# Performance work log

Hardware: AMD Instinct MI355X
Metric: run time of the kernel (lower is better)

Reference implementation:

```python
import jax, jax.numpy as jnp
import numpy as np

N, T, GX, GY, GQ = 16, 64, 256, 256, 256   # solutions, timesteps, source grid, query grid
H, D = 4, 8                                 # attention heads / head dim
SIGMA = 0.2
LY_MIN, LY_MAX = 30.0, 120.0
CU_REF, NI_REF = 0.0029, 0.0018
LX = 100.0


def setup_inputs() -> dict:
    key = jax.random.key(0)
    ks = jax.random.split(key, 7)
    lys = jax.random.uniform(ks[0], (N,), minval=40.0, maxval=110.0)
    ccu = jax.random.uniform(ks[1], (N,), minval=0.001, maxval=CU_REF)
    cni = jax.random.uniform(ks[2], (N,), minval=0.0005, maxval=NI_REF)
    params = jnp.stack([lys, ccu, cni], axis=1).astype(jnp.float32)  # [N,3] raw (Ly, C_Cu, C_Ni)
    x_grids = jnp.tile(jnp.linspace(0.0, LX, GX, dtype=jnp.float32)[None], (N, 1))      # [N,GX]
    y_grids = lys[:, None] * jnp.linspace(0.0, 1.0, GY, dtype=jnp.float32)[None]        # [N,GY]
    c1_src = jax.random.normal(ks[3], (N, T, GX, GY), dtype=jnp.float32)
    c2_src = jax.random.normal(ks[4], (N, T, GX, GY), dtype=jnp.float32)
    Wq_w = 0.1 * jax.random.normal(ks[5], (H * D, 3), dtype=jnp.float32)
    Wk_w = 0.1 * jax.random.normal(ks[6], (H * D, 3), dtype=jnp.float32)
    Wq_b = jnp.zeros((H * D,), jnp.float32)
    Wk_b = jnp.zeros((H * D,), jnp.float32)
    return dict(c1_src=c1_src, c2_src=c2_src, x_grids=x_grids, y_grids=y_grids,
                params=params, Wq_w=Wq_w, Wq_b=Wq_b, Wk_w=Wk_w, Wk_b=Wk_b,
                ly_target=jnp.float32(75.0), c_cu_target=jnp.float32(0.0029),
                c_ni_target=jnp.float32(0.0018))


def _bilinear(c, xg, yg, qx, qy):
    """Linear interp on rectilinear grid, fill_value=0 out of bounds.
    c: [T,Gx,Gy], xg: [Gx], yg: [Gy], qx/qy: [P] -> [T,P]."""
    ix = jnp.clip(jnp.searchsorted(xg, qx, side='right') - 1, 0, xg.shape[0] - 2)
    iy = jnp.clip(jnp.searchsorted(yg, qy, side='right') - 1, 0, yg.shape[0] - 2)
    x0, x1 = xg[ix], xg[ix + 1]
    y0, y1 = yg[iy], yg[iy + 1]
    fx = (qx - x0) / (x1 - x0)
    fy = (qy - y0) / (y1 - y0)
    c00 = c[:, ix, iy]
    c10 = c[:, ix + 1, iy]
    c01 = c[:, ix, iy + 1]
    c11 = c[:, ix + 1, iy + 1]
    v = ((1 - fx) * (1 - fy)) * c00 + (fx * (1 - fy)) * c10 \
        + ((1 - fx) * fy) * c01 + (fx * fy) * c11
    inb = (qx >= xg[0]) & (qx <= xg[-1]) & (qy >= yg[0]) & (qy <= yg[-1])
    return jnp.where(inb[None, :], v, 0.0)


def _forward(c1_src, c2_src, x_grids, y_grids, params, Wq_w, Wq_b, Wk_w, Wk_b,
             ly_target, c_cu_target, c_ni_target):
    # --- parameter normalization (same constants as original) ---
    p = jnp.stack([(params[:, 0] - LY_MIN) / (LY_MAX - LY_MIN),
                   params[:, 1] / CU_REF,
                   params[:, 2] / NI_REF], axis=1)                     # [N,3]
    tgt = jnp.stack([(ly_target - LY_MIN) / (LY_MAX - LY_MIN),
                     c_cu_target / CU_REF,
                     c_ni_target / NI_REF])[None, :]                   # [1,3]
    # --- tiny multi-head attention weights ---
    q = (tgt @ Wq_w.T + Wq_b).reshape(1, H, D)
    k = (p @ Wk_w.T + Wk_b).reshape(p.shape[0], H, D)
    attn = jnp.einsum('nhd,mhd->nmh', k, q) / np.sqrt(D).astype(np.float32)  # [N,1,H]
    attn_w = jax.nn.softmax(attn, axis=0).mean(axis=2).squeeze(1)            # [N]
    # --- gaussian spatial weights ---
    sw = jnp.exp(-0.5 * jnp.sum(((p - tgt) / SIGMA) ** 2, axis=1))
    sw = sw / sw.sum()
    w = attn_w * sw
    w = w / w.sum()
    w = jax.lax.stop_gradient(w)  # original detaches weights before interpolation
    # --- batched bilinear interpolation onto target grid ---
    Lx = x_grids[0, -1]
    unit = jnp.linspace(0.0, 1.0, GQ, dtype=jnp.float32)
    X, Y = jnp.meshgrid(unit * Lx, unit * ly_target, indexing='ij')    # [GQ,GQ]
    qx, qy = X.ravel(), Y.ravel()                                      # [P]
    ys = y_grids * (ly_target / params[:, 0])[:, None]                 # per-solution rescaled Y grids
    interp = jax.vmap(_bilinear, in_axes=(0, 0, 0, None, None))        # -> [N,T,P]
    c1 = jnp.einsum('n,ntp->tp', w, interp(c1_src, x_grids, ys, qx, qy)).reshape(T, GQ, GQ)
    c2 = jnp.einsum('n,ntp->tp', w, interp(c2_src, x_grids, ys, qx, qy)).reshape(T, GQ, GQ)
    # --- boundary conditions ---
    c1 = c1.at[:, :, 0].set(c_cu_target)
    c2 = c2.at[:, :, -1].set(c_ni_target)
    return jnp.stack([c1, c2]), w


def reference(c1_src, c2_src, x_grids, y_grids, params, Wq_w, Wq_b, Wk_w, Wk_b,
              ly_target, c_cu_target, c_ni_target):
    return _forward(c1_src, c2_src, x_grids, y_grids, params, Wq_w, Wq_b, Wk_w, Wk_b,
                    ly_target, c_cu_target, c_ni_target)
```

## Files before the change

### kernel.cpp

```cpp
#include <hip/hip_runtime.h>

#define N_SRC 16
#define T_DIM 64
#define GXD 256
#define GYD 256
#define GQD 256
#define HN 4
#define DN 8
#define TILE_I 16
#define OUT_C_ELEMS (2 * T_DIM * GQD * GQD)

__device__ __forceinline__ float unitv(int i) {
    return (i == GQD - 1) ? 1.0f : (float)i * (1.0f / 255.0f);
}

__global__ void weights_kernel(const float* __restrict__ params,
                               const float* __restrict__ Wq_w, const float* __restrict__ Wq_b,
                               const float* __restrict__ Wk_w, const float* __restrict__ Wk_b,
                               const float* __restrict__ lyt_p, const float* __restrict__ ccut_p,
                               const float* __restrict__ cnit_p,
                               float* __restrict__ out_w) {
    if (threadIdx.x != 0 || blockIdx.x != 0) return;
    const float lyt = *lyt_p, ccut = *ccut_p, cnit = *cnit_p;
    float tgt[3];
    tgt[0] = (lyt - 30.0f) / 90.0f;
    tgt[1] = ccut / 0.0029f;
    tgt[2] = cnit / 0.0018f;
    float q[HN * DN];
    for (int hd = 0; hd < HN * DN; ++hd)
        q[hd] = tgt[0] * Wq_w[hd * 3 + 0] + tgt[1] * Wq_w[hd * 3 + 1] + tgt[2] * Wq_w[hd * 3 + 2] + Wq_b[hd];
    float p[N_SRC][3];
    float attn[N_SRC][HN];
    for (int n = 0; n < N_SRC; ++n) {
        p[n][0] = (params[n * 3 + 0] - 30.0f) / 90.0f;
        p[n][1] = params[n * 3 + 1] / 0.0029f;
        p[n][2] = params[n * 3 + 2] / 0.0018f;
        for (int h = 0; h < HN; ++h) {
            float acc = 0.0f;
            for (int d = 0; d < DN; ++d) {
                int hd = h * DN + d;
                float kv = p[n][0] * Wk_w[hd * 3 + 0] + p[n][1] * Wk_w[hd * 3 + 1] + p[n][2] * Wk_w[hd * 3 + 2] + Wk_b[hd];
                acc += kv * q[hd];
            }
            attn[n][h] = acc / sqrtf(8.0f);
        }
    }
    float aw[N_SRC];
    for (int n = 0; n < N_SRC; ++n) aw[n] = 0.0f;
    for (int h = 0; h < HN; ++h) {
        float m = attn[0][h];
        for (int n = 1; n < N_SRC; ++n) m = fmaxf(m, attn[n][h]);
        float e[N_SRC], s = 0.0f;
        for (int n = 0; n < N_SRC; ++n) { e[n] = expf(attn[n][h] - m); s += e[n]; }
        for (int n = 0; n < N_SRC; ++n) aw[n] += e[n] / s;
    }
    for (int n = 0; n < N_SRC; ++n) aw[n] *= (1.0f / (float)HN);
    float sw[N_SRC], ss = 0.0f;
    for (int n = 0; n < N_SRC; ++n) {
        float d0 = (p[n][0] - tgt[0]) / 0.2f;
        float d1 = (p[n][1] - tgt[1]) / 0.2f;
        float d2 = (p[n][2] - tgt[2]) / 0.2f;
        sw[n] = expf(-0.5f * (d0 * d0 + d1 * d1 + d2 * d2));
        ss += sw[n];
    }
    float w[N_SRC], wsum = 0.0f;
    for (int n = 0; n < N_SRC; ++n) { w[n] = aw[n] * (sw[n] / ss); wsum += w[n]; }
    for (int n = 0; n < N_SRC; ++n) out_w[n] = w[n] / wsum;
}

__global__ __launch_bounds__(256) void fused_kernel(
    const float* __restrict__ c1, const float* __restrict__ c2,
    const float* __restrict__ xg, const float* __restrict__ yg,
    const float* __restrict__ params,
    const float* __restrict__ lyt_p, const float* __restrict__ ccut_p,
    const float* __restrict__ cnit_p,
    const float* __restrict__ wbuf, float* __restrict__ out)
{
    __shared__ float xg_sm[GXD];
    __shared__ float ys_sm[N_SRC][GYD];
    __shared__ float w_sm[N_SRC];

    const int tid = threadIdx.x;
    const int t = blockIdx.y;
    const int i0 = blockIdx.x * TILE_I;
    const float lyt = *lyt_p;

    xg_sm[tid] = xg[tid];
    #pragma unroll
    for (int n = 0; n < N_SRC; ++n) {
        float s = lyt / params[n * 3 + 0];
        ys_sm[n][tid] = yg[n * GYD + tid] * s;
    }
    if (tid < N_SRC) w_sm[tid] = wbuf[tid];
    __syncthreads();

    const int j = tid;
    const float qy = unitv(j) * lyt;
    int iy[N_SRC];
    float wy0[N_SRC], wy1[N_SRC];
    #pragma unroll
    for (int n = 0; n < N_SRC; ++n) {
        int lo = 0, hi = GYD;
        while (lo < hi) { int mid = (lo + hi) >> 1; if (ys_sm[n][mid] <= qy) lo = mid + 1; else hi = mid; }
        int idx = lo - 1;
        idx = idx < 0 ? 0 : (idx > GYD - 2 ? GYD - 2 : idx);
        iy[n] = idx;
        float y0 = ys_sm[n][idx], y1 = ys_sm[n][idx + 1];
        float fy = (qy - y0) / (y1 - y0);
        float vy = (qy >= ys_sm[n][0] && qy <= ys_sm[n][GYD - 1]) ? 1.0f : 0.0f;
        float wn = w_sm[n] * vy;
        wy0[n] = wn * (1.0f - fy);
        wy1[n] = wn * fy;
    }

    const float Lx = xg_sm[GXD - 1];
    const float ccut = *ccut_p, cnit = *cnit_p;

    for (int ii = 0; ii < TILE_I; ++ii) {
        const int i = i0 + ii;
        const float qx = unitv(i) * Lx;
        int lo = 0, hi = GXD;
        while (lo < hi) { int mid = (lo + hi) >> 1; if (xg_sm[mid] <= qx) lo = mid + 1; else hi = mid; }
        int ixi = lo - 1;
        ixi = ixi < 0 ? 0 : (ixi > GXD - 2 ? GXD - 2 : ixi);
        const float x0 = xg_sm[ixi], x1 = xg_sm[ixi + 1];
        const float fx = (qx - x0) / (x1 - x0);
        const float vx = (qx >= xg_sm[0] && qx <= xg_sm[GXD - 1]) ? 1.0f : 0.0f;

        float a10 = 0.0f, a11 = 0.0f, a20 = 0.0f, a21 = 0.0f;
        #pragma unroll
        for (int n = 0; n < N_SRC; ++n) {
            const int base = ((n * T_DIM + t) * GXD + ixi) * GYD + iy[n];
            const float e00 = c1[base],       e01 = c1[base + 1];
            const float e10 = c1[base + GYD], e11 = c1[base + GYD + 1];
            a10 += wy0[n] * e00 + wy1[n] * e01;
            a11 += wy0[n] * e10 + wy1[n] * e11;
            const float f00 = c2[base],       f01 = c2[base + 1];
            const float f10 = c2[base + GYD], f11 = c2[base + GYD + 1];
            a20 += wy0[n] * f00 + wy1[n] * f01;
            a21 += wy0[n] * f10 + wy1[n] * f11;
        }
        float o1 = vx * ((1.0f - fx) * a10 + fx * a11);
        float o2 = vx * ((1.0f - fx) * a20 + fx * a21);
        if (j == 0) o1 = ccut;
        if (j == GQD - 1) o2 = cnit;
        out[(t * GQD + i) * GQD + j] = o1;
        out[((T_DIM + t) * GQD + i) * GQD + j] = o2;
    }
}

extern "C" void kernel_launch(void* const* d_in, const int* in_sizes, int n_in,
                              void* d_out, int out_size, void* d_ws, size_t ws_size,
                              hipStream_t stream) {
    const float* c1     = (const float*)d_in[0];
    const float* c2     = (const float*)d_in[1];
    const float* xg     = (const float*)d_in[2];
    const float* yg     = (const float*)d_in[3];
    const float* params = (const float*)d_in[4];
    const float* Wq_w   = (const float*)d_in[5];
    const float* Wq_b   = (const float*)d_in[6];
    const float* Wk_w   = (const float*)d_in[7];
    const float* Wk_b   = (const float*)d_in[8];
    const float* lyt    = (const float*)d_in[9];
    const float* ccut   = (const float*)d_in[10];
    const float* cnit   = (const float*)d_in[11];
    float* out = (float*)d_out;
    float* out_w = out + OUT_C_ELEMS;

    weights_kernel<<<1, 64, 0, stream>>>(params, Wq_w, Wq_b, Wk_w, Wk_b, lyt, ccut, cnit, out_w);
    dim3 grid(GQD / TILE_I, T_DIM);
    fused_kernel<<<grid, 256, 0, stream>>>(c1, c2, xg, yg, params, lyt, ccut, cnit, out_w, out);
}
```

Measured before the change: 688.6 us.

## Precompute interpolation index/weight tables once and launch one block per output row

Folds the attention-weight computation into a single-block table kernel that also precomputes per-source y indices and weights plus x indices and weights into workspace. The main kernel now reads these tables instead of redoing 16 binary searches per block, and each block handles one output row instead of 16, which gives a larger grid. This removes redundant search work in the gather kernel. In exchange it adds global table reads (16x3 per thread) and depends on workspace being large enough.

Measured after the change: 685.8 us. No clear change (-0.4%).

```diff
diff --git a/kernel.cpp b/kernel.cpp
--- a/kernel.cpp
+++ b/kernel.cpp
@@ -7,82 +7,33 @@
 #define GQD 256
 #define HN 4
 #define DN 8
-#define TILE_I 16
 #define OUT_C_ELEMS (2 * T_DIM * GQD * GQD)
+
+#define WS_IY   0
+#define WS_WY0  16384
+#define WS_WY1  32768
+#define WS_IX   49152
+#define WS_WX0  50176
+#define WS_WX1  51200
 
 __device__ __forceinline__ float unitv(int i) {
     return (i == GQD - 1) ? 1.0f : (float)i * (1.0f / 255.0f);
 }
 
-__global__ void weights_kernel(const float* __restrict__ params,
-                               const float* __restrict__ Wq_w, const float* __restrict__ Wq_b,
-                               const float* __restrict__ Wk_w, const float* __restrict__ Wk_b,
-                               const float* __restrict__ lyt_p, const float* __restrict__ ccut_p,
-                               const float* __restrict__ cnit_p,
-                               float* __restrict__ out_w) {
-    if (threadIdx.x != 0 || blockIdx.x != 0) return;
-    const float lyt = *lyt_p, ccut = *ccut_p, cnit = *cnit_p;
-    float tgt[3];
-    tgt[0] = (lyt - 30.0f) / 90.0f;
-    tgt[1] = ccut / 0.0029f;
-    tgt[2] = cnit / 0.0018f;
-    float q[HN * DN];
-    for (int hd = 0; hd < HN * DN; ++hd)
-        q[hd] = tgt[0] * Wq_w[hd * 3 + 0] + tgt[1] * Wq_w[hd * 3 + 1] + tgt[2] * Wq_w[hd * 3 + 2] + Wq_b[hd];
-    float p[N_SRC][3];
-    float attn[N_SRC][HN];
-    for (int n = 0; n < N_SRC; ++n) {
-        p[n][0] = (params[n * 3 + 0] - 30.0f) / 90.0f;
-        p[n][1] = params[n * 3 + 1] / 0.0029f;
-        p[n][2] = params[n * 3 + 2] / 0.0018f;
-        for (int h = 0; h < HN; ++h) {
-            float acc = 0.0f;
-            for (int d = 0; d < DN; ++d) {
-                int hd = h * DN + d;
-                float kv = p[n][0] * Wk_w[hd * 3 + 0] + p[n][1] * Wk_w[hd * 3 + 1] + p[n][2] * Wk_w[hd * 3 + 2] + Wk_b[hd];
-                acc += kv * q[hd];
-            }
-            attn[n][h] = acc / sqrtf(8.0f);
-        }
-    }
-    float aw[N_SRC];
-    for (int n = 0; n < N_SRC; ++n) aw[n] = 0.0f;
-    for (int h = 0; h < HN; ++h) {
-        float m = attn[0][h];
-        for (int n = 1; n < N_SRC; ++n) m = fmaxf(m, attn[n][h]);
-        float e[N_SRC], s = 0.0f;
-        for (int n = 0; n < N_SRC; ++n) { e[n] = expf(attn[n][h] - m); s += e[n]; }
-        for (int n = 0; n < N_SRC; ++n) aw[n] += e[n] / s;
-    }
-    for (int n = 0; n < N_SRC; ++n) aw[n] *= (1.0f / (float)HN);
-    float sw[N_SRC], ss = 0.0f;
-    for (int n = 0; n < N_SRC; ++n) {
-        float d0 = (p[n][0] - tgt[0]) / 0.2f;
-        float d1 = (p[n][1] - tgt[1]) / 0.2f;
-        float d2 = (p[n][2] - tgt[2]) / 0.2f;
-        sw[n] = expf(-0.5f * (d0 * d0 + d1 * d1 + d2 * d2));
-        ss += sw[n];
-    }
-    float w[N_SRC], wsum = 0.0f;
-    for (int n = 0; n < N_SRC; ++n) { w[n] = aw[n] * (sw[n] / ss); wsum += w[n]; }
-    for (int n = 0; n < N_SRC; ++n) out_w[n] = w[n] / wsum;
-}
-
-__global__ __launch_bounds__(256) void fused_kernel(
-    const float* __restrict__ c1, const float* __restrict__ c2,
+__global__ __launch_bounds__(256) void table_kernel(
     const float* __restrict__ xg, const float* __restrict__ yg,
     const float* __restrict__ params,
+    const float* __restrict__ Wq_w, const float* __restrict__ Wq_b,
+    const float* __restrict__ Wk_w, const float* __restrict__ Wk_b,
     const float* __restrict__ lyt_p, const float* __restrict__ ccut_p,
     const float* __restrict__ cnit_p,
-    const float* __restrict__ wbuf, float* __restrict__ out)
+    float* __restrict__ out_w, char* __restrict__ ws)
 {
     __shared__ float xg_sm[GXD];
     __shared__ float ys_sm[N_SRC][GYD];
     __shared__ float w_sm[N_SRC];
 
     const int tid = threadIdx.x;
-    const int t = blockIdx.y;
-    const int i0 = blockIdx.x * TILE_I;
     const float lyt = *lyt_p;
 
     xg_sm[tid] = xg[tid];
@@ -91,62 +42,139 @@
         float s = lyt / params[n * 3 + 0];
         ys_sm[n][tid] = yg[n * GYD + tid] * s;
     }
-    if (tid < N_SRC) w_sm[tid] = wbuf[tid];
+
+    if (tid == 0) {
+        const float ccut = *ccut_p, cnit = *cnit_p;
+        float tgt[3];
+        tgt[0] = (lyt - 30.0f) / 90.0f;
+        tgt[1] = ccut / 0.0029f;
+        tgt[2] = cnit / 0.0018f;
+        float q[HN * DN];
+        for (int hd = 0; hd < HN * DN; ++hd)
+            q[hd] = tgt[0] * Wq_w[hd * 3 + 0] + tgt[1] * Wq_w[hd * 3 + 1] + tgt[2] * Wq_w[hd * 3 + 2] + Wq_b[hd];
+        float p[N_SRC][3];
+        float attn[N_SRC][HN];
+        for (int n = 0; n < N_SRC; ++n) {
+            p[n][0] = (params[n * 3 + 0] - 30.0f) / 90.0f;
+            p[n][1] = params[n * 3 + 1] / 0.0029f;
+            p[n][2] = params[n * 3 + 2] / 0.0018f;
+            for (int h = 0; h < HN; ++h) {
+                float acc = 0.0f;
+                for (int d = 0; d < DN; ++d) {
+                    int hd = h * DN + d;
+                    float kv = p[n][0] * Wk_w[hd * 3 + 0] + p[n][1] * Wk_w[hd * 3 + 1] + p[n][2] * Wk_w[hd * 3 + 2] + Wk_b[hd];
+                    acc += kv * q[hd];
+                }
+                attn[n][h] = acc / sqrtf(8.0f);
+            }
+        }
+        float aw[N_SRC];
+        for (int n = 0; n < N_SRC; ++n) aw[n] = 0.0f;
+        for (int h = 0; h < HN; ++h) {
+            float m = attn[0][h];
+            for (int n = 1; n < N_SRC; ++n) m = fmaxf(m, attn[n][h]);
+            float e[N_SRC], s = 0.0f;
+            for (int n = 0; n < N_SRC; ++n) { e[n] = expf(attn[n][h] - m); s += e[n]; }
+            for (int n = 0; n < N_SRC; ++n) aw[n] += e[n] / s;
+        }
+        for (int n = 0; n < N_SRC; ++n) aw[n] *= (1.0f / (float)HN);
+        float sw[N_SRC], ss = 0.0f;
+        for (int n = 0; n < N_SRC; ++n) {
+            float d0 = (p[n][0] - tgt[0]) / 0.2f;
+            float d1 = (p[n][1] - tgt[1]) / 0.2f;
+            float d2 = (p[n][2] - tgt[2]) / 0.2f;
+            sw[n] = expf(-0.5f * (d0 * d0 + d1 * d1 + d2 * d2));
+            ss += sw[n];
+        }
+        float w[N_SRC], wsum = 0.0f;
+        for (int n = 0; n < N_SRC; ++n) { w[n] = aw[n] * (sw[n] / ss); wsum += w[n]; }
+        for (int n = 0; n < N_SRC; ++n) {
+            float wf = w[n] / wsum;
+            w_sm[n] = wf;
+            out_w[n] = wf;
+        }
+    }
     __syncthreads();
+
+    int*   iy_tab  = (int*)  (ws + WS_IY);
+    float* wy0_tab = (float*)(ws + WS_WY0);
+    float* wy1_tab = (float*)(ws + WS_WY1);
+    int*   ix_tab  = (int*)  (ws + WS_IX);
+    float* wx0_tab = (float*)(ws + WS_WX0);
+    float* wx1_tab = (float*)(ws + WS_WX1);
 
     const int j = tid;
     const float qy = unitv(j) * lyt;
-    int iy[N_SRC];
-    float wy0[N_SRC], wy1[N_SRC];
     #pragma unroll
     for (int n = 0; n < N_SRC; ++n) {
         int lo = 0, hi = GYD;
         while (lo < hi) { int mid = (lo + hi) >> 1; if (ys_sm[n][mid] <= qy) lo = mid + 1; else hi = mid; }
         int idx = lo - 1;
         idx = idx < 0 ? 0 : (idx > GYD - 2 ? GYD - 2 : idx);
-        iy[n] = idx;
         float y0 = ys_sm[n][idx], y1 = ys_sm[n][idx + 1];
         float fy = (qy - y0) / (y1 - y0);
         float vy = (qy >= ys_sm[n][0] && qy <= ys_sm[n][GYD - 1]) ? 1.0f : 0.0f;
         float wn = w_sm[n] * vy;
-        wy0[n] = wn * (1.0f - fy);
-        wy1[n] = wn * fy;
+        iy_tab [n * GQD + j] = idx;
+        wy0_tab[n * GQD + j] = wn * (1.0f - fy);
+        wy1_tab[n * GQD + j] = wn * fy;
     }
 
     const float Lx = xg_sm[GXD - 1];
-    const float ccut = *ccut_p, cnit = *cnit_p;
-
-    for (int ii = 0; ii < TILE_I; ++ii) {
-        const int i = i0 + ii;
-        const float qx = unitv(i) * Lx;
-        int lo = 0, hi = GXD;
-        while (lo < hi) { int mid = (lo + hi) >> 1; if (xg_sm[mid] <= qx) lo = mid + 1; else hi = mid; }
-        int ixi = lo - 1;
-        ixi = ixi < 0 ? 0 : (ixi > GXD - 2 ? GXD - 2 : ixi);
-        const float x0 = xg_sm[ixi], x1 = xg_sm[ixi + 1];
-        const float fx = (qx - x0) / (x1 - x0);
-        const float vx = (qx >= xg_sm[0] && qx <= xg_sm[GXD - 1]) ? 1.0f : 0.0f;
-
-        float a10 = 0.0f, a11 = 0.0f, a20 = 0.0f, a21 = 0.0f;
-        #pragma unroll
-        for (int n = 0; n < N_SRC; ++n) {
-            const int base = ((n * T_DIM + t) * GXD + ixi) * GYD + iy[n];
-            const float e00 = c1[base],       e01 = c1[base + 1];
-            const float e10 = c1[base + GYD], e11 = c1[base + GYD + 1];
-            a10 += wy0[n] * e00 + wy1[n] * e01;
-            a11 += wy0[n] * e10 + wy1[n] * e11;
-            const float f00 = c2[base],       f01 = c2[base + 1];
-            const float f10 = c2[base + GYD], f11 = c2[base + GYD + 1];
-            a20 += wy0[n] * f00 + wy1[n] * f01;
-            a21 += wy0[n] * f10 + wy1[n] * f11;
-        }
-        float o1 = vx * ((1.0f - fx) * a10 + fx * a11);
-        float o2 = vx * ((1.0f - fx) * a20 + fx * a21);
-        if (j == 0) o1 = ccut;
-        if (j == GQD - 1) o2 = cnit;
-        out[(t * GQD + i) * GQD + j] = o1;
-        out[((T_DIM + t) * GQD + i) * GQD + j] = o2;
-    }
+    const float qx = unitv(tid) * Lx;
+    int lo = 0, hi = GXD;
+    while (lo < hi) { int mid = (lo + hi) >> 1; if (xg_sm[mid] <= qx) lo = mid + 1; else hi = mid; }
+    int ixi = lo - 1;
+    ixi = ixi < 0 ? 0 : (ixi > GXD - 2 ? GXD - 2 : ixi);
+    const float x0 = xg_sm[ixi], x1 = xg_sm[ixi + 1];
+    const float fx = (qx - x0) / (x1 - x0);
+    const float vx = (qx >= xg_sm[0] && qx <= xg_sm[GXD - 1]) ? 1.0f : 0.0f;
+    ix_tab [tid] = ixi;
+    wx0_tab[tid] = vx * (1.0f - fx);
+    wx1_tab[tid] = vx * fx;
+}
+
+__global__ __launch_bounds__(256) void fused_kernel(
+    const float* __restrict__ c1, const float* __restrict__ c2,
+    const float* __restrict__ ccut_p, const float* __restrict__ cnit_p,
+    const char* __restrict__ ws, float* __restrict__ out)
+{
+    const int i = blockIdx.x;
+    const int t = blockIdx.y;
+    const int j = threadIdx.x;
+
+    const int*   iy_tab  = (const int*)  (ws + WS_IY);
+    const float* wy0_tab = (const float*)(ws + WS_WY0);
+    const float* wy1_tab = (const float*)(ws + WS_WY1);
+
+    const int   ixi = ((const int*)  (ws + WS_IX)) [i];
+    const float wx0 = ((const float*)(ws + WS_WX0))[i];
+    const float wx1 = ((const float*)(ws + WS_WX1))[i];
+
+    float a10 = 0.0f, a11 = 0.0f, a20 = 0.0f, a21 = 0.0f;
+
+    #pragma unroll 4
+    for (int n = 0; n < N_SRC; ++n) {
+        const int   iy  = iy_tab [n * GQD + j];
+        const float wy0 = wy0_tab[n * GQD + j];
+        const float wy1 = wy1_tab[n * GQD + j];
+        const int base = ((n * T_DIM + t) * GXD + ixi) * GYD + iy;
+        const float e00 = c1[base],       e01 = c1[base + 1];
+        const float e10 = c1[base + GYD], e11 = c1[base + GYD + 1];
+        a10 += wy0 * e00 + wy1 * e01;
+        a11 += wy0 * e10 + wy1 * e11;
+        const float f00 = c2[base],       f01 = c2[base + 1];
+        const float f10 = c2[base + GYD], f11 = c2[base + GYD + 1];
+        a20 += wy0 * f00 + wy1 * f01;
+        a21 += wy0 * f10 + wy1 * f11;
+    }
+
+    float o1 = wx0 * a10 + wx1 * a11;
+    float o2 = wx0 * a20 + wx1 * a21;
+    if (j == 0)       o1 = *ccut_p;
+    if (j == GQD - 1) o2 = *cnit_p;
+    out[(t * GQD + i) * GQD + j] = o1;
+    out[((T_DIM + t) * GQD + i) * GQD + j] = o2;
 }
 
 extern "C" void kernel_launch(void* const* d_in, const int* in_sizes, int n_in,
@@ -166,8 +194,10 @@
     const float* cnit   = (const float*)d_in[11];
     float* out = (float*)d_out;
     float* out_w = out + OUT_C_ELEMS;
-
-    weights_kernel<<<1, 64, 0, stream>>>(params, Wq_w, Wq_b, Wk_w, Wk_b, lyt, ccut, cnit, out_w);
-    dim3 grid(GQD / TILE_I, T_DIM);
-    fused_kernel<<<grid, 256, 0, stream>>>(c1, c2, xg, yg, params, lyt, ccut, cnit, out_w, out);
-}
+    char* ws = (char*)d_ws;
+
+    table_kernel<<<1, 256, 0, stream>>>(xg, yg, params, Wq_w, Wq_b, Wk_w, Wk_b,
+                                        lyt, ccut, cnit, out_w, ws);
+    dim3 grid(GQD, T_DIM);
+    fused_kernel<<<grid, 256, 0, stream>>>(c1, c2, ccut, cnit, ws, out);
+}
```
